# Kernel optimization log

Hardware: AMD Instinct MI355X
Metric: run time of the kernel (lower is better)

## Reference

```python
import jax, jax.numpy as jnp
import numpy as np

# 3x3 window roll offsets, row-major as in PatchShift2D.shift_content
SHIFTS = [(1, 1), (1, 0), (1, -1), (0, 1), (0, 0), (0, -1), (-1, 1), (-1, 0), (-1, -1)]
NUM_WIN = 9


def patch_shift(x, inv):
    # x: [B, T, H, W, C]; pad C up to multiple of 9 and H,W by 1, roll each
    # of the 9 channel groups by a distinct (h, w) offset, then crop back.
    B, T, H, W, C = x.shape
    Ch = int(np.ceil(C / NUM_WIN) * NUM_WIN)
    xp = jnp.pad(x, ((0, 0), (0, 0), (1, 1), (1, 1), (0, Ch - C)))
    m = -1 if inv else 1
    parts = jnp.split(xp, NUM_WIN, axis=-1)
    shifted = [jnp.roll(p, (m * sh, m * sw), axis=(2, 3))
               for p, (sh, sw) in zip(parts, SHIFTS)]
    return jnp.concatenate(shifted, axis=-1)[:, :, 1:H + 1, 1:W + 1, :C]


def _gelu(v):
    return jax.nn.gelu(v, approximate=False)  # torch nn.GELU default (erf)


def setup_inputs() -> dict:
    key = jax.random.key(0)
    ks = jax.random.split(key, 14)
    B, T, H, W, C = 2, 8, 56, 56, 512
    HID = 1024
    s = 0.02
    return {
        "x": jax.random.normal(ks[0], (B, T, H, W, C), dtype=jnp.float32),
        "fc_w": s * jax.random.normal(ks[1], (C, HID), dtype=jnp.float32),
        "fc_b": jnp.zeros((HID,), jnp.float32),
        "fc1_w": s * jax.random.normal(ks[2], (HID, C), dtype=jnp.float32),
        "fc1_b": jnp.zeros((C,), jnp.float32),
        "fc2_w": s * jax.random.normal(ks[3], (HID, C), dtype=jnp.float32),
        "fc2_b": jnp.zeros((C,), jnp.float32),
        "rw1_w": s * jax.random.normal(ks[4], (C, C // 4), dtype=jnp.float32),
        "rw1_b": jnp.zeros((C // 4,), jnp.float32),
        "rw2_w": s * jax.random.normal(ks[5], (C // 4, 2 * C), dtype=jnp.float32),
        "rw2_b": jnp.zeros((2 * C,), jnp.float32),
        "proj_w": s * jax.random.normal(ks[6], (C, C), dtype=jnp.float32),
        "proj_b": jnp.zeros((C,), jnp.float32),
    }


def reference(x, fc_w, fc_b, fc1_w, fc1_b, fc2_w, fc2_b,
              rw1_w, rw1_b, rw2_w, rw2_b, proj_w, proj_b):
    B, T, H, W, C = x.shape
    xh = _gelu(x @ fc_w + fc_b)                                  # [B,T,H,W,HID]
    h = patch_shift(_gelu(patch_shift(xh, False) @ fc1_w + fc1_b), True)  # [B,T,H,W,C]
    w = _gelu(xh @ fc2_w + fc2_b)                                 # [B,T,H,W,C]
    a = (h + w).mean(axis=(1, 2, 3))                              # [B,C]
    a = _gelu(a @ rw1_w + rw1_b) @ rw2_w + rw2_b                  # [B,2C]
    a = jax.nn.softmax(a.reshape(B, C, 2).transpose(2, 0, 1), axis=0)  # [2,B,C]
    a = a[:, :, None, None, None, :]                              # [2,B,1,1,1,C]
    out = h * a[0] + w * a[1]
    return out @ proj_w + proj_b
```

## Files before the change

kernel.cpp:

```cpp
#include <hip/hip_runtime.h>
#include <hip/hip_bf16.h>
#include <stdint.h>


typedef __attribute__((ext_vector_type(8))) short short8;
typedef __attribute__((ext_vector_type(4))) float floatx4;
typedef unsigned int uint;
typedef unsigned short ushort;

#define NTOK   50176
#define HWIMG  3136

__device__ __forceinline__ float gelu_exact(float v) {
    return 0.5f * v * (1.0f + erff(v * 0.70710678118654752440f));
}
__device__ __forceinline__ float gelu_fast(float v) {
    float u = v * (0.7978845608f + 0.0356774081f * v * v);
    return v * __builtin_amdgcn_rcpf(1.0f + __expf(-2.0f * u));
}

__device__ __forceinline__ int shift_h(int g) { return 1 - g / 3; }
__device__ __forceinline__ int shift_w(int g) { return 1 - g % 3; }

typedef const __attribute__((address_space(1))) uint* gas_ptr;
typedef __attribute__((address_space(3))) uint* las_ptr;

__device__ __forceinline__ void async_copy16(const void* g, void* l) {
    gas_ptr gp = (gas_ptr)(uintptr_t)g;
    las_ptr lp = (las_ptr)(uint32_t)(uintptr_t)l;
    __builtin_amdgcn_global_load_lds(gp, lp, 16, 0, 0);
}

template <int EPI, bool SHIFTA>
__global__ __launch_bounds__(256) void gemm_bt(
    const __hip_bfloat16* __restrict__ A,
    const __hip_bfloat16* __restrict__ Bt,
    const float* __restrict__ bias,
    void* __restrict__ Cout,
    float* __restrict__ ssum, int N, int K)
{
    __shared__ __align__(16) __hip_bfloat16 As[128 * 32];
    __shared__ __align__(16) __hip_bfloat16 Bs[128 * 32];

    const int t    = threadIdx.x;
    const int lane = t & 63;
    const int wave = t >> 6;
    const int wm   = wave >> 1;
    const int wn   = wave & 1;

    const int nbn  = gridDim.x;
    const int flat = blockIdx.y * nbn + blockIdx.x;
    const int xcd  = flat & 7;
    const int j    = flat >> 3;
    const int jd   = j / nbn;
    const int bm   = xcd * 49 + jd;
    const int bn   = j - jd * nbn;

    const int ar0 = bm * 128 + (t >> 2);
    const int ar1 = ar0 + 64;
    const int ac  = (t & 3) * 8;

    const __hip_bfloat16* ga0 = A  + (size_t)ar0 * K + ac;
    const __hip_bfloat16* ga1 = ga0 + (size_t)64 * K;
    const __hip_bfloat16* gb0 = Bt + (size_t)(bn * 128 + (t >> 2)) * K + ac;
    const __hip_bfloat16* gb1 = gb0 + (size_t)64 * K;
    __hip_bfloat16* la0 = &As[t * 8];
    __hip_bfloat16* la1 = &As[t * 8 + 2048];
    __hip_bfloat16* lb0 = &Bs[t * 8];
    __hip_bfloat16* lb1 = &Bs[t * 8 + 2048];

    int oh0 = 0, ow0 = 0, oh1 = 0, ow1 = 0;
    if (SHIFTA) {
        const int rem0 = ar0 % HWIMG, rem1 = ar1 % HWIMG;
        oh0 = rem0 / 56; ow0 = rem0 - oh0 * 56;
        oh1 = rem1 / 56; ow1 = rem1 - oh1 * 56;
    }

    floatx4 acc[4][4] = {};

    const int kq = (lane >> 4) * 8;
    const int ml = lane & 15;

    for (int k0 = 0; k0 < K; k0 += 32) {
        async_copy16(gb0, lb0);
        async_copy16(gb1, lb1);
        gb0 += 32; gb1 += 32;

        uint4 av0 = {0, 0, 0, 0}, av1 = {0, 0, 0, 0};
        if (SHIFTA) {
            const int c0 = k0 + ac;
            const int g  = c0 / 114;
            const int ge = (c0 + 7) / 114;
            if (g == ge) {
                const int sh = shift_h(g), sw = shift_w(g);
                const int off = sh * 56 + sw;
                if ((unsigned)(oh0 - sh) < 56u && (unsigned)(ow0 - sw) < 56u)
                    av0 = *(const uint4*)(A + (size_t)(ar0 - off) * K + c0);
                if ((unsigned)(oh1 - sh) < 56u && (unsigned)(ow1 - sw) < 56u)
                    av1 = *(const uint4*)(A + (size_t)(ar1 - off) * K + c0);
            } else {
                union { ushort us[8]; uint4 v; } p0, p1;
#pragma unroll
                for (int e = 0; e < 8; e++) {
                    const int c  = c0 + e;
                    const int gg = c / 114;
                    const int sh = shift_h(gg), sw = shift_w(gg);
                    const int off = sh * 56 + sw;
                    ushort v0 = 0, v1 = 0;
                    if ((unsigned)(oh0 - sh) < 56u && (unsigned)(ow0 - sw) < 56u)
                        v0 = *(const ushort*)(A + (size_t)(ar0 - off) * K + c);
                    if ((unsigned)(oh1 - sh) < 56u && (unsigned)(ow1 - sw) < 56u)
                        v1 = *(const ushort*)(A + (size_t)(ar1 - off) * K + c);
                    p0.us[e] = v0; p1.us[e] = v1;
                }
                av0 = p0.v; av1 = p1.v;
            }
        } else {
            async_copy16(ga0, la0);
            async_copy16(ga1, la1);
            ga0 += 32; ga1 += 32;
        }

        asm volatile("s_waitcnt vmcnt(0)" ::: "memory");
        if (SHIFTA) {
            *(uint4*)la0 = av0;
            *(uint4*)la1 = av1;
        }
        __syncthreads();

        short8 af[4], bf[4];
#pragma unroll
        for (int i = 0; i < 4; i++) {
            af[i] = *(const short8*)&As[(wm * 64 + i * 16 + ml) * 32 + kq];
            bf[i] = *(const short8*)&Bs[(wn * 64 + i * 16 + ml) * 32 + kq];
        }
#pragma unroll
        for (int mi = 0; mi < 4; mi++)
#pragma unroll
            for (int ni = 0; ni < 4; ni++)
                acc[mi][ni] = __builtin_amdgcn_mfma_f32_16x16x32_bf16(
                    af[mi], bf[ni], acc[mi][ni], 0, 0, 0);
        __syncthreads();
    }

    const int rq = (lane >> 4) * 4;

    int cols[4], gsh[4], gsw[4];
    float bv[4];
    float sum[4] = {0.f, 0.f, 0.f, 0.f};
#pragma unroll
    for (int ni = 0; ni < 4; ni++) {
        const int col = bn * 128 + wn * 64 + ni * 16 + ml;
        cols[ni] = col;
        bv[ni] = bias[col];
        if (EPI == 2) { const int g = col / 57; gsh[ni] = shift_h(g); gsw[ni] = shift_w(g); }
    }

#pragma unroll
    for (int mi = 0; mi < 4; mi++) {
        const int row0 = bm * 128 + wm * 64 + mi * 16 + rq;
        int phr[4], pwr[4];
        if (EPI == 2) {
            const int bt_ = row0 / HWIMG;
            const int rem = row0 - bt_ * HWIMG;
            const int ph0 = rem / 56;
            const int pw0 = rem - ph0 * 56;
#pragma unroll
            for (int r = 0; r < 4; r++) {
                int pw = pw0 + r, ph = ph0;
                if (pw >= 56) { pw -= 56; ph += 1; }
                if (ph >= 56) { ph = 0; }
                phr[r] = ph; pwr[r] = pw;
            }
        }
#pragma unroll
        for (int ni = 0; ni < 4; ni++) {
            const int col = cols[ni];
#pragma unroll
            for (int r = 0; r < 4; r++) {
                const int tok = row0 + r;
                float v = acc[mi][ni][r] + bv[ni];
                if (EPI != 0) v = gelu_fast(v);
                if (EPI == 0) {
                    ((float*)Cout)[(size_t)tok * N + col] = v;
                } else if (EPI == 1) {
                    ((__hip_bfloat16*)Cout)[(size_t)tok * N + col] = __float2bfloat16(v);
                } else if (EPI == 2) {
                    const int th = phr[r] - gsh[ni], tw = pwr[r] - gsw[ni];
                    if ((unsigned)th < 56u && (unsigned)tw < 56u) {
                        ((__hip_bfloat16*)Cout)[(size_t)(tok - gsh[ni] * 56 - gsw[ni]) * N + col]
                            = __float2bfloat16(v);
                        sum[ni] += v;
                    }
                } else {
                    ((__hip_bfloat16*)Cout)[(size_t)tok * N + col] = __float2bfloat16(v);
                    sum[ni] += v;
                }
            }
        }
    }

    if (EPI == 2 || EPI == 3) {
        const int b = (bm >= 196) ? 1 : 0;
#pragma unroll
        for (int ni = 0; ni < 4; ni++) {
            float s = sum[ni];
            s += __shfl_xor(s, 16, 64);
            s += __shfl_xor(s, 32, 64);
            if (lane < 16) atomicAdd(&ssum[b * 512 + cols[ni]], s);
        }
    }
}

template <int C, int GS, int SGN>
__global__ __launch_bounds__(256) void zero_holes(__hip_bfloat16* __restrict__ buf)
{
    const int i = blockIdx.x * 256 + threadIdx.x;
    const int c = i % C;
    const int p = i / C;
    const int bt = p / 220, fp = p % 220;
    int oh, ow;
    if (fp < 56)       { oh = 0;        ow = fp; }
    else if (fp < 112) { oh = 55;       ow = fp - 56; }
    else if (fp < 166) { oh = fp - 111; ow = 0; }
    else               { oh = fp - 165; ow = 55; }
    const int g = c / GS;
    const int ih = oh - SGN * shift_h(g);
    const int iw = ow - SGN * shift_w(g);
    if ((unsigned)ih >= 56u || (unsigned)iw >= 56u)
        buf[((size_t)(bt * HWIMG + oh * 56 + ow)) * C + c] = __float2bfloat16(0.0f);
}

__global__ __launch_bounds__(256) void cvt_x(const float4* __restrict__ x,
                                             __hip_bfloat16* __restrict__ xb)
{
    int i = blockIdx.x * 256 + threadIdx.x;
    float4 v = x[i];
    __hip_bfloat16 b0 = __float2bfloat16(v.x);
    __hip_bfloat16 b1 = __float2bfloat16(v.y);
    __hip_bfloat16 b2 = __float2bfloat16(v.z);
    __hip_bfloat16 b3 = __float2bfloat16(v.w);
    uint2 o;
    o.x = (uint)*(ushort*)&b0 | ((uint)*(ushort*)&b1 << 16);
    o.y = (uint)*(ushort*)&b2 | ((uint)*(ushort*)&b3 << 16);
    *(uint2*)&xb[(size_t)i * 4] = o;
}

__global__ __launch_bounds__(256) void prep_w(
    const float* __restrict__ fcw,  const float* __restrict__ fc1w,
    const float* __restrict__ fc2w, const float* __restrict__ projw,
    __hip_bfloat16* __restrict__ fcwT, __hip_bfloat16* __restrict__ fc1T,
    __hip_bfloat16* __restrict__ fc2T, __hip_bfloat16* __restrict__ projT)
{
    int i = blockIdx.x * 256 + threadIdx.x;
    if (i < 524288) {
        int n = i >> 9, k = i & 511;
        fcwT[i] = __float2bfloat16(fcw[k * 1024 + n]);
    } else if (i < 1048576) {
        int j = i - 524288;
        int n = j >> 10, k = j & 1023;
        fc1T[j] = __float2bfloat16(fc1w[k * 512 + n]);
    } else if (i < 1572864) {
        int j = i - 1048576;
        int n = j >> 10, k = j & 1023;
        fc2T[j] = __float2bfloat16(fc2w[k * 512 + n]);
    } else if (i < 1835008) {
        int j = i - 1572864;
        int n = j >> 9, k = j & 511;
        projT[j] = __float2bfloat16(projw[k * 512 + n]);
    }
}

__global__ __launch_bounds__(256) void tiny_mlp(
    const float* __restrict__ s0, const float* __restrict__ s1,
    const float* __restrict__ rw1_w, const float* __restrict__ rw1_b,
    const float* __restrict__ rw2_w, const float* __restrict__ rw2_b,
    float* __restrict__ a0, float* __restrict__ a1)
{
    __shared__ float mean[1024];
    __shared__ float z[256];
    __shared__ float av[2048];
    const int t = threadIdx.x;
    for (int i = t; i < 1024; i += 256)
        mean[i] = (s0[i] + s1[i]) * (1.0f / 25088.0f);
    __syncthreads();
    {
        const int b = t >> 7, j = t & 127;
        float acc = rw1_b[j];
        for (int cc = 0; cc < 512; cc++)
            acc += mean[b * 512 + cc] * rw1_w[cc * 128 + j];
        z[t] = gelu_exact(acc);
    }
    __syncthreads();
    for (int i = t; i < 2048; i += 256) {
        const int b = i >> 10, o = i & 1023;
        float acc = rw2_b[o];
        for (int j = 0; j < 128; j++)
            acc += z[b * 128 + j] * rw2_w[j * 1024 + o];
        av[i] = acc;
    }
    __syncthreads();
    for (int i = t; i < 1024; i += 256) {
        const int b = i >> 9, cc = i & 511;
        const float x0 = av[b * 1024 + 2 * cc];
        const float x1 = av[b * 1024 + 2 * cc + 1];
        const float m = fmaxf(x0, x1);
        const float e0 = expf(x0 - m), e1 = expf(x1 - m);
        const float inv = 1.0f / (e0 + e1);
        a0[i] = e0 * inv;
        a1[i] = e1 * inv;
    }
}

__device__ __forceinline__ float bf_lo(uint u) { return __uint_as_float(u << 16); }
__device__ __forceinline__ float bf_hi(uint u) { return __uint_as_float(u & 0xffff0000u); }
__device__ __forceinline__ uint pack_bf2(float lo, float hi) {
    __hip_bfloat16 a = __float2bfloat16(lo), b = __float2bfloat16(hi);
    return (uint)*(ushort*)&a | ((uint)*(ushort*)&b << 16);
}

__global__ __launch_bounds__(256) void combine(
    const uint4* __restrict__ hs4, const uint4* __restrict__ w4,
    const float* __restrict__ a0, const float* __restrict__ a1,
    uint4* __restrict__ hw4)
{
    const int i = blockIdx.x * 256 + threadIdx.x;
    const int ck = i & 63;
    const int tok = i >> 6;
    const int b = (tok >= 25088) ? 1 : 0;
    const float4* A0 = (const float4*)&a0[b * 512 + ck * 8];
    const float4* A1 = (const float4*)&a1[b * 512 + ck * 8];
    const float4 s0l = A0[0], s0h = A0[1];
    const float4 s1l = A1[0], s1h = A1[1];
    const uint4 h = hs4[i], w = w4[i];
    uint4 o;
    o.x = pack_bf2(bf_lo(h.x) * s0l.x + bf_lo(w.x) * s1l.x,
                   bf_hi(h.x) * s0l.y + bf_hi(w.x) * s1l.y);
    o.y = pack_bf2(bf_lo(h.y) * s0l.z + bf_lo(w.y) * s1l.z,
                   bf_hi(h.y) * s0l.w + bf_hi(w.y) * s1l.w);
    o.z = pack_bf2(bf_lo(h.z) * s0h.x + bf_lo(w.z) * s1h.x,
                   bf_hi(h.z) * s0h.y + bf_hi(w.z) * s1h.y);
    o.w = pack_bf2(bf_lo(h.w) * s0h.z + bf_lo(w.w) * s1h.z,
                   bf_hi(h.w) * s0h.w + bf_hi(w.w) * s1h.w);
    hw4[i] = o;
}

extern "C" void kernel_launch(void* const* d_in, const int* in_sizes, int n_in,
                              void* d_out, int out_size, void* d_ws, size_t ws_size,
                              hipStream_t stream)
{
    const float* x      = (const float*)d_in[0];
    const float* fc_w   = (const float*)d_in[1];
    const float* fc_b   = (const float*)d_in[2];
    const float* fc1_w  = (const float*)d_in[3];
    const float* fc1_b  = (const float*)d_in[4];
    const float* fc2_w  = (const float*)d_in[5];
    const float* fc2_b  = (const float*)d_in[6];
    const float* rw1_w  = (const float*)d_in[7];
    const float* rw1_b  = (const float*)d_in[8];
    const float* rw2_w  = (const float*)d_in[9];
    const float* rw2_b  = (const float*)d_in[10];
    const float* proj_w = (const float*)d_in[11];
    const float* proj_b = (const float*)d_in[12];

    uint8_t* ws = (uint8_t*)d_ws;
    __hip_bfloat16* xh  = (__hip_bfloat16*)(ws);
    __hip_bfloat16* xb  = (__hip_bfloat16*)(ws + 102760448);
    uint8_t* wt         = ws + 102760448 + 51380224;
    __hip_bfloat16* fcwT  = (__hip_bfloat16*)(wt);
    __hip_bfloat16* fc1T  = fcwT + 524288;
    __hip_bfloat16* fc2T  = fc1T + 524288;
    __hip_bfloat16* projT = fc2T + 524288;
    float* s0 = (float*)(wt + 3670016);
    float* s1 = s0 + 1024;
    float* a0 = s1 + 1024;
    float* a1 = a0 + 1024;

    __hip_bfloat16* wbuf = (__hip_bfloat16*)d_out;
    __hip_bfloat16* hs   = xb;
    __hip_bfloat16* hw   = xh;

    hipMemsetAsync(s0, 0, 8192, stream);

    cvt_x<<<25088, 256, 0, stream>>>((const float4*)x, xb);
    prep_w<<<7168, 256, 0, stream>>>(fc_w, fc1_w, fc2_w, proj_w, fcwT, fc1T, fc2T, projT);

    gemm_bt<1, false><<<dim3(8, 392), 256, 0, stream>>>(xb, fcwT, fc_b, xh, nullptr, 1024, 512);
    zero_holes<512, 57, -1><<<7040, 256, 0, stream>>>(hs);
    gemm_bt<2, true><<<dim3(4, 392), 256, 0, stream>>>(xh, fc1T, fc1_b, hs, s0, 512, 1024);
    gemm_bt<3, false><<<dim3(4, 392), 256, 0, stream>>>(xh, fc2T, fc2_b, wbuf, s1, 512, 1024);
    tiny_mlp<<<1, 256, 0, stream>>>(s0, s1, rw1_w, rw1_b, rw2_w, rw2_b, a0, a1);
    combine<<<12544, 256, 0, stream>>>((const uint4*)hs, (const uint4*)wbuf, a0, a1, (uint4*)hw);
    gemm_bt<0, false><<<dim3(4, 392), 256, 0, stream>>>(hw, projT, proj_b, d_out, nullptr, 512, 512);
}
```

Measured before the change: 621.3 us.

## Fuse fc1 and fc2 GEMMs into one kernel sharing the xh tile reads

Merges the shifted-A fc1 GEMM and the plain fc2 GEMM into a single kernel that loads the same xh rows once per k-step, in both shifted and unshifted form, and keeps two accumulator sets. The goal is to avoid reading the large xh activation twice from memory and to drop one launch. The cost is doubled accumulator registers (32 floatx4) and doubled LDS per block, which may lower occupancy or cause spills.

```diff
diff --git a/kernel.cpp b/kernel.cpp
--- a/kernel.cpp
+++ b/kernel.cpp
@@ -31,13 +31,12 @@
     __builtin_amdgcn_global_load_lds(gp, lp, 16, 0, 0);
 }
 
-template <int EPI, bool SHIFTA>
+template <int EPI>
 __global__ __launch_bounds__(256) void gemm_bt(
     const __hip_bfloat16* __restrict__ A,
     const __hip_bfloat16* __restrict__ Bt,
     const float* __restrict__ bias,
-    void* __restrict__ Cout,
-    float* __restrict__ ssum, int N, int K)
+    void* __restrict__ Cout, int N, int K)
 {
     __shared__ __align__(16) __hip_bfloat16 As[128 * 32];
     __shared__ __align__(16) __hip_bfloat16 Bs[128 * 32];
@@ -56,38 +55,128 @@
     const int bm   = xcd * 49 + jd;
     const int bn   = j - jd * nbn;
 
-    const int ar0 = bm * 128 + (t >> 2);
-    const int ar1 = ar0 + 64;
-    const int ac  = (t & 3) * 8;
-
-    const __hip_bfloat16* ga0 = A  + (size_t)ar0 * K + ac;
+    const __hip_bfloat16* ga0 = A  + (size_t)(bm * 128 + (t >> 2)) * K + (t & 3) * 8;
     const __hip_bfloat16* ga1 = ga0 + (size_t)64 * K;
-    const __hip_bfloat16* gb0 = Bt + (size_t)(bn * 128 + (t >> 2)) * K + ac;
+    const __hip_bfloat16* gb0 = Bt + (size_t)(bn * 128 + (t >> 2)) * K + (t & 3) * 8;
     const __hip_bfloat16* gb1 = gb0 + (size_t)64 * K;
     __hip_bfloat16* la0 = &As[t * 8];
     __hip_bfloat16* la1 = &As[t * 8 + 2048];
     __hip_bfloat16* lb0 = &Bs[t * 8];
     __hip_bfloat16* lb1 = &Bs[t * 8 + 2048];
 
-    int oh0 = 0, ow0 = 0, oh1 = 0, ow1 = 0;
-    if (SHIFTA) {
-        const int rem0 = ar0 % HWIMG, rem1 = ar1 % HWIMG;
-        oh0 = rem0 / 56; ow0 = rem0 - oh0 * 56;
-        oh1 = rem1 / 56; ow1 = rem1 - oh1 * 56;
-    }
-
     floatx4 acc[4][4] = {};
 
     const int kq = (lane >> 4) * 8;
     const int ml = lane & 15;
 
     for (int k0 = 0; k0 < K; k0 += 32) {
+        async_copy16(ga0, la0);
+        async_copy16(ga1, la1);
         async_copy16(gb0, lb0);
         async_copy16(gb1, lb1);
-        gb0 += 32; gb1 += 32;
+        ga0 += 32; ga1 += 32; gb0 += 32; gb1 += 32;
+        asm volatile("s_waitcnt vmcnt(0)" ::: "memory");
+        __syncthreads();
+
+        short8 af[4], bf[4];
+#pragma unroll
+        for (int i = 0; i < 4; i++) {
+            af[i] = *(const short8*)&As[(wm * 64 + i * 16 + ml) * 32 + kq];
+            bf[i] = *(const short8*)&Bs[(wn * 64 + i * 16 + ml) * 32 + kq];
+        }
+#pragma unroll
+        for (int mi = 0; mi < 4; mi++)
+#pragma unroll
+            for (int ni = 0; ni < 4; ni++)
+                acc[mi][ni] = __builtin_amdgcn_mfma_f32_16x16x32_bf16(
+                    af[mi], bf[ni], acc[mi][ni], 0, 0, 0);
+        __syncthreads();
+    }
+
+    const int rq = (lane >> 4) * 4;
+
+#pragma unroll
+    for (int mi = 0; mi < 4; mi++) {
+        const int row0 = bm * 128 + wm * 64 + mi * 16 + rq;
+#pragma unroll
+        for (int ni = 0; ni < 4; ni++) {
+            const int col = bn * 128 + wn * 64 + ni * 16 + ml;
+            const float bv = bias[col];
+#pragma unroll
+            for (int r = 0; r < 4; r++) {
+                const int tok = row0 + r;
+                float v = acc[mi][ni][r] + bv;
+                if (EPI == 0) {
+                    ((float*)Cout)[(size_t)tok * N + col] = v;
+                } else {
+                    v = gelu_fast(v);
+                    ((__hip_bfloat16*)Cout)[(size_t)tok * N + col] = __float2bfloat16(v);
+                }
+            }
+        }
+    }
+}
+
+__global__ __launch_bounds__(256) void gemm23(
+    const __hip_bfloat16* __restrict__ A,
+    const __hip_bfloat16* __restrict__ B1t,
+    const __hip_bfloat16* __restrict__ B2t,
+    const float* __restrict__ bias1, const float* __restrict__ bias2,
+    __hip_bfloat16* __restrict__ C1, __hip_bfloat16* __restrict__ C2,
+    float* __restrict__ s0, float* __restrict__ s1)
+{
+    const int N = 512, K = 1024;
+    __shared__ __align__(16) __hip_bfloat16 Ash[128 * 32];
+    __shared__ __align__(16) __hip_bfloat16 Aun[128 * 32];
+    __shared__ __align__(16) __hip_bfloat16 B1s[128 * 32];
+    __shared__ __align__(16) __hip_bfloat16 B2s[128 * 32];
+
+    const int t    = threadIdx.x;
+    const int lane = t & 63;
+    const int wave = t >> 6;
+    const int wm   = wave >> 1;
+    const int wn   = wave & 1;
+
+    const int nbn  = gridDim.x;
+    const int flat = blockIdx.y * nbn + blockIdx.x;
+    const int xcd  = flat & 7;
+    const int j    = flat >> 3;
+    const int jd   = j / nbn;
+    const int bm   = xcd * 49 + jd;
+    const int bn   = j - jd * nbn;
+
+    const int ar0 = bm * 128 + (t >> 2);
+    const int ar1 = ar0 + 64;
+    const int ac  = (t & 3) * 8;
+
+    const __hip_bfloat16* gau0 = A   + (size_t)ar0 * K + ac;
+    const __hip_bfloat16* gau1 = gau0 + (size_t)64 * K;
+    const __hip_bfloat16* gb10 = B1t + (size_t)(bn * 128 + (t >> 2)) * K + ac;
+    const __hip_bfloat16* gb11 = gb10 + (size_t)64 * K;
+    const __hip_bfloat16* gb20 = B2t + (size_t)(bn * 128 + (t >> 2)) * K + ac;
+    const __hip_bfloat16* gb21 = gb20 + (size_t)64 * K;
+
+    const int rem0 = ar0 % HWIMG, rem1 = ar1 % HWIMG;
+    const int oh0 = rem0 / 56, ow0 = rem0 - oh0 * 56;
+    const int oh1 = rem1 / 56, ow1 = rem1 - oh1 * 56;
+
+    floatx4 acch[4][4] = {};
+    floatx4 accw[4][4] = {};
+
+    const int kq = (lane >> 4) * 8;
+    const int ml = lane & 15;
+
+    for (int k0 = 0; k0 < K; k0 += 32) {
+        async_copy16(gau0, &Aun[t * 8]);
+        async_copy16(gau1, &Aun[t * 8 + 2048]);
+        async_copy16(gb10, &B1s[t * 8]);
+        async_copy16(gb11, &B1s[t * 8 + 2048]);
+        async_copy16(gb20, &B2s[t * 8]);
+        async_copy16(gb21, &B2s[t * 8 + 2048]);
+        gau0 += 32; gau1 += 32; gb10 += 32; gb11 += 32; gb20 += 32; gb21 += 32;
 
         uint4 av0 = {0, 0, 0, 0}, av1 = {0, 0, 0, 0};
-        if (SHIFTA) {
+        {
             const int c0 = k0 + ac;
             const int g  = c0 / 114;
             const int ge = (c0 + 7) / 114;
@@ -115,63 +204,65 @@
                 }
                 av0 = p0.v; av1 = p1.v;
             }
-        } else {
-            async_copy16(ga0, la0);
-            async_copy16(ga1, la1);
-            ga0 += 32; ga1 += 32;
         }
 
         asm volatile("s_waitcnt vmcnt(0)" ::: "memory");
-        if (SHIFTA) {
-            *(uint4*)la0 = av0;
-            *(uint4*)la1 = av1;
-        }
+        *(uint4*)&Ash[t * 8] = av0;
+        *(uint4*)&Ash[t * 8 + 2048] = av1;
         __syncthreads();
 
-        short8 af[4], bf[4];
+        short8 afs[4], afu[4], bf1[4], bf2[4];
 #pragma unroll
         for (int i = 0; i < 4; i++) {
-            af[i] = *(const short8*)&As[(wm * 64 + i * 16 + ml) * 32 + kq];
-            bf[i] = *(const short8*)&Bs[(wn * 64 + i * 16 + ml) * 32 + kq];
+            const int arow = (wm * 64 + i * 16 + ml) * 32 + kq;
+            const int brow = (wn * 64 + i * 16 + ml) * 32 + kq;
+            afs[i] = *(const short8*)&Ash[arow];
+            afu[i] = *(const short8*)&Aun[arow];
+            bf1[i] = *(const short8*)&B1s[brow];
+            bf2[i] = *(const short8*)&B2s[brow];
         }
 #pragma unroll
         for (int mi = 0; mi < 4; mi++)
 #pragma unroll
-            for (int ni = 0; ni < 4; ni++)
-                acc[mi][ni] = __builtin_amdgcn_mfma_f32_16x16x32_bf16(
-                    af[mi], bf[ni], acc[mi][ni], 0, 0, 0);
+            for (int ni = 0; ni < 4; ni++) {
+                acch[mi][ni] = __builtin_amdgcn_mfma_f32_16x16x32_bf16(
+                    afs[mi], bf1[ni], acch[mi][ni], 0, 0, 0);
+                accw[mi][ni] = __builtin_amdgcn_mfma_f32_16x16x32_bf16(
+                    afu[mi], bf2[ni], accw[mi][ni], 0, 0, 0);
+            }
         __syncthreads();
     }
 
     const int rq = (lane >> 4) * 4;
 
     int cols[4], gsh[4], gsw[4];
-    float bv[4];
-    float sum[4] = {0.f, 0.f, 0.f, 0.f};
+    float bv1[4], bv2[4];
+    float sumh[4] = {0.f, 0.f, 0.f, 0.f};
+    float sumw[4] = {0.f, 0.f, 0.f, 0.f};
 #pragma unroll
     for (int ni = 0; ni < 4; ni++) {
         const int col = bn * 128 + wn * 64 + ni * 16 + ml;
         cols[ni] = col;
-        bv[ni] = bias[col];
-        if (EPI == 2) { const int g = col / 57; gsh[ni] = shift_h(g); gsw[ni] = shift_w(g); }
+        bv1[ni] = bias1[col];
+        bv2[ni] = bias2[col];
+        const int g = col / 57;
+        gsh[ni] = shift_h(g); gsw[ni] = shift_w(g);
     }
 
 #pragma unroll
     for (int mi = 0; mi < 4; mi++) {
         const int row0 = bm * 128 + wm * 64 + mi * 16 + rq;
+        const int bt_ = row0 / HWIMG;
+        const int rem = row0 - bt_ * HWIMG;
+        const int ph0 = rem / 56;
+        const int pw0 = rem - ph0 * 56;
         int phr[4], pwr[4];
-        if (EPI == 2) {
-            const int bt_ = row0 / HWIMG;
-            const int rem = row0 - bt_ * HWIMG;
-            const int ph0 = rem / 56;
-            const int pw0 = rem - ph0 * 56;
-#pragma unroll
-            for (int r = 0; r < 4; r++) {
-                int pw = pw0 + r, ph = ph0;
-                if (pw >= 56) { pw -= 56; ph += 1; }
-                if (ph >= 56) { ph = 0; }
-                phr[r] = ph; pwr[r] = pw;
-            }
+#pragma unroll
+        for (int r = 0; r < 4; r++) {
+            int pw = pw0 + r, ph = ph0;
+            if (pw >= 56) { pw -= 56; ph += 1; }
+            if (ph >= 56) { ph = 0; }
+            phr[r] = ph; pwr[r] = pw;
         }
 #pragma unroll
         for (int ni = 0; ni < 4; ni++) {
@@ -179,35 +270,32 @@
 #pragma unroll
             for (int r = 0; r < 4; r++) {
                 const int tok = row0 + r;
-                float v = acc[mi][ni][r] + bv[ni];
-                if (EPI != 0) v = gelu_fast(v);
-                if (EPI == 0) {
-                    ((float*)Cout)[(size_t)tok * N + col] = v;
-                } else if (EPI == 1) {
-                    ((__hip_bfloat16*)Cout)[(size_t)tok * N + col] = __float2bfloat16(v);
-                } else if (EPI == 2) {
-                    const int th = phr[r] - gsh[ni], tw = pwr[r] - gsw[ni];
-                    if ((unsigned)th < 56u && (unsigned)tw < 56u) {
-                        ((__hip_bfloat16*)Cout)[(size_t)(tok - gsh[ni] * 56 - gsw[ni]) * N + col]
-                            = __float2bfloat16(v);
-                        sum[ni] += v;
-                    }
-                } else {
-                    ((__hip_bfloat16*)Cout)[(size_t)tok * N + col] = __float2bfloat16(v);
-                    sum[ni] += v;
+                float vw = gelu_fast(accw[mi][ni][r] + bv2[ni]);
+                C2[(size_t)tok * N + col] = __float2bfloat16(vw);
+                sumw[ni] += vw;
+                float vh = gelu_fast(acch[mi][ni][r] + bv1[ni]);
+                const int th = phr[r] - gsh[ni], tw = pwr[r] - gsw[ni];
+                if ((unsigned)th < 56u && (unsigned)tw < 56u) {
+                    C1[(size_t)(tok - gsh[ni] * 56 - gsw[ni]) * N + col]
+                        = __float2bfloat16(vh);
+                    sumh[ni] += vh;
                 }
             }
         }
     }
 
-    if (EPI == 2 || EPI == 3) {
-        const int b = (bm >= 196) ? 1 : 0;
-#pragma unroll
-        for (int ni = 0; ni < 4; ni++) {
-            float s = sum[ni];
-            s += __shfl_xor(s, 16, 64);
-            s += __shfl_xor(s, 32, 64);
-            if (lane < 16) atomicAdd(&ssum[b * 512 + cols[ni]], s);
+    const int b = (bm >= 196) ? 1 : 0;
+#pragma unroll
+    for (int ni = 0; ni < 4; ni++) {
+        float sh_ = sumh[ni];
+        sh_ += __shfl_xor(sh_, 16, 64);
+        sh_ += __shfl_xor(sh_, 32, 64);
+        float sw_ = sumw[ni];
+        sw_ += __shfl_xor(sw_, 16, 64);
+        sw_ += __shfl_xor(sw_, 32, 64);
+        if (lane < 16) {
+            atomicAdd(&s0[b * 512 + cols[ni]], sh_);
+            atomicAdd(&s1[b * 512 + cols[ni]], sw_);
         }
     }
 }
@@ -385,11 +473,11 @@
     cvt_x<<<25088, 256, 0, stream>>>((const float4*)x, xb);
     prep_w<<<7168, 256, 0, stream>>>(fc_w, fc1_w, fc2_w, proj_w, fcwT, fc1T, fc2T, projT);
 
-    gemm_bt<1, false><<<dim3(8, 392), 256, 0, stream>>>(xb, fcwT, fc_b, xh, nullptr, 1024, 512);
+    gemm_bt<1><<<dim3(8, 392), 256, 0, stream>>>(xb, fcwT, fc_b, xh, 1024, 512);
     zero_holes<512, 57, -1><<<7040, 256, 0, stream>>>(hs);
-    gemm_bt<2, true><<<dim3(4, 392), 256, 0, stream>>>(xh, fc1T, fc1_b, hs, s0, 512, 1024);
-    gemm_bt<3, false><<<dim3(4, 392), 256, 0, stream>>>(xh, fc2T, fc2_b, wbuf, s1, 512, 1024);
+    gemm23<<<dim3(4, 392), 256, 0, stream>>>(xh, fc1T, fc2T, fc1_b, fc2_b,
+                                             hs, wbuf, s0, s1);
     tiny_mlp<<<1, 256, 0, stream>>>(s0, s1, rw1_w, rw1_b, rw2_w, rw2_b, a0, a1);
     combine<<<12544, 256, 0, stream>>>((const uint4*)hs, (const uint4*)wbuf, a0, a1, (uint4*)hw);
-    gemm_bt<0, false><<<dim3(4, 392), 256, 0, stream>>>(hw, projT, proj_b, d_out, nullptr, 512, 512);
-}
+    gemm_bt<0><<<dim3(4, 392), 256, 0, stream>>>(hw, projT, proj_b, d_out, 512, 512);
+}
```

Measured after the change: 742.6 us. +19.5%, slower.

## Fuse input bf16 conversion and attention combine into GEMM A-operand loads

Applied to the files above, without the earlier changes.

The first GEMM now reads fp32 x directly and converts it to bf16 while staging into LDS, removing the separate conversion kernel and its intermediate buffer. When the workspace is large enough, the final projection GEMM builds its A tile on the fly as h*a0 + w*a1 from the two branch outputs, eliminating the combine kernel and the hw buffer round trip. Both paths replace async global-to-LDS copies with register loads plus ALU work, which may reduce load/compute overlap inside those GEMMs.

```diff
diff --git a/kernel.cpp b/kernel.cpp
--- a/kernel.cpp
+++ b/kernel.cpp
@@ -22,6 +22,13 @@
 __device__ __forceinline__ int shift_h(int g) { return 1 - g / 3; }
 __device__ __forceinline__ int shift_w(int g) { return 1 - g % 3; }
 
+__device__ __forceinline__ float bf_lo(uint u) { return __uint_as_float(u << 16); }
+__device__ __forceinline__ float bf_hi(uint u) { return __uint_as_float(u & 0xffff0000u); }
+__device__ __forceinline__ uint pack_bf2(float lo, float hi) {
+    __hip_bfloat16 a = __float2bfloat16(lo), b = __float2bfloat16(hi);
+    return (uint)*(ushort*)&a | ((uint)*(ushort*)&b << 16);
+}
+
 typedef const __attribute__((address_space(1))) uint* gas_ptr;
 typedef __attribute__((address_space(3))) uint* las_ptr;
 
@@ -31,11 +38,14 @@
     __builtin_amdgcn_global_load_lds(gp, lp, 16, 0, 0);
 }
 
-template <int EPI, bool SHIFTA>
+template <int EPI, int ASRC>
 __global__ __launch_bounds__(256) void gemm_bt(
-    const __hip_bfloat16* __restrict__ A,
+    const void* __restrict__ Av,
+    const __hip_bfloat16* __restrict__ A2,
     const __hip_bfloat16* __restrict__ Bt,
     const float* __restrict__ bias,
+    const float* __restrict__ sc0,
+    const float* __restrict__ sc1,
     void* __restrict__ Cout,
     float* __restrict__ ssum, int N, int K)
 {
@@ -56,11 +66,14 @@
     const int bm   = xcd * 49 + jd;
     const int bn   = j - jd * nbn;
 
+    const __hip_bfloat16* Ab = (const __hip_bfloat16*)Av;
+    const float*          Af = (const float*)Av;
+
     const int ar0 = bm * 128 + (t >> 2);
     const int ar1 = ar0 + 64;
     const int ac  = (t & 3) * 8;
 
-    const __hip_bfloat16* ga0 = A  + (size_t)ar0 * K + ac;
+    const __hip_bfloat16* ga0 = Ab + (size_t)ar0 * K + ac;
     const __hip_bfloat16* ga1 = ga0 + (size_t)64 * K;
     const __hip_bfloat16* gb0 = Bt + (size_t)(bn * 128 + (t >> 2)) * K + ac;
     const __hip_bfloat16* gb1 = gb0 + (size_t)64 * K;
@@ -70,11 +83,12 @@
     __hip_bfloat16* lb1 = &Bs[t * 8 + 2048];
 
     int oh0 = 0, ow0 = 0, oh1 = 0, ow1 = 0;
-    if (SHIFTA) {
+    if (ASRC == 3) {
         const int rem0 = ar0 % HWIMG, rem1 = ar1 % HWIMG;
         oh0 = rem0 / 56; ow0 = rem0 - oh0 * 56;
         oh1 = rem1 / 56; ow1 = rem1 - oh1 * 56;
     }
+    const int bsel = (ASRC == 2 && bm >= 196) ? 1 : 0;
 
     floatx4 acc[4][4] = {};
 
@@ -87,7 +101,46 @@
         gb0 += 32; gb1 += 32;
 
         uint4 av0 = {0, 0, 0, 0}, av1 = {0, 0, 0, 0};
-        if (SHIFTA) {
+        if (ASRC == 0) {
+            async_copy16(ga0, la0);
+            async_copy16(ga1, la1);
+            ga0 += 32; ga1 += 32;
+        } else if (ASRC == 1) {
+            const float* p0 = Af + (size_t)ar0 * K + k0 + ac;
+            const float* p1 = Af + (size_t)ar1 * K + k0 + ac;
+            const float4 f0 = *(const float4*)p0, f1 = *(const float4*)(p0 + 4);
+            const float4 f2 = *(const float4*)p1, f3 = *(const float4*)(p1 + 4);
+            av0.x = pack_bf2(f0.x, f0.y); av0.y = pack_bf2(f0.z, f0.w);
+            av0.z = pack_bf2(f1.x, f1.y); av0.w = pack_bf2(f1.z, f1.w);
+            av1.x = pack_bf2(f2.x, f2.y); av1.y = pack_bf2(f2.z, f2.w);
+            av1.z = pack_bf2(f3.x, f3.y); av1.w = pack_bf2(f3.z, f3.w);
+        } else if (ASRC == 2) {
+            const int c0 = k0 + ac;
+            const float4 s0l = *(const float4*)&sc0[bsel * 512 + c0];
+            const float4 s0h = *(const float4*)&sc0[bsel * 512 + c0 + 4];
+            const float4 s1l = *(const float4*)&sc1[bsel * 512 + c0];
+            const float4 s1h = *(const float4*)&sc1[bsel * 512 + c0 + 4];
+            const uint4 h0 = *(const uint4*)(Ab + (size_t)ar0 * K + c0);
+            const uint4 w0 = *(const uint4*)(A2 + (size_t)ar0 * K + c0);
+            const uint4 h1 = *(const uint4*)(Ab + (size_t)ar1 * K + c0);
+            const uint4 w1 = *(const uint4*)(A2 + (size_t)ar1 * K + c0);
+            av0.x = pack_bf2(bf_lo(h0.x) * s0l.x + bf_lo(w0.x) * s1l.x,
+                             bf_hi(h0.x) * s0l.y + bf_hi(w0.x) * s1l.y);
+            av0.y = pack_bf2(bf_lo(h0.y) * s0l.z + bf_lo(w0.y) * s1l.z,
+                             bf_hi(h0.y) * s0l.w + bf_hi(w0.y) * s1l.w);
+            av0.z = pack_bf2(bf_lo(h0.z) * s0h.x + bf_lo(w0.z) * s1h.x,
+                             bf_hi(h0.z) * s0h.y + bf_hi(w0.z) * s1h.y);
+            av0.w = pack_bf2(bf_lo(h0.w) * s0h.z + bf_lo(w0.w) * s1h.z,
+                             bf_hi(h0.w) * s0h.w + bf_hi(w0.w) * s1h.w);
+            av1.x = pack_bf2(bf_lo(h1.x) * s0l.x + bf_lo(w1.x) * s1l.x,
+                             bf_hi(h1.x) * s0l.y + bf_hi(w1.x) * s1l.y);
+            av1.y = pack_bf2(bf_lo(h1.y) * s0l.z + bf_lo(w1.y) * s1l.z,
+                             bf_hi(h1.y) * s0l.w + bf_hi(w1.y) * s1l.w);
+            av1.z = pack_bf2(bf_lo(h1.z) * s0h.x + bf_lo(w1.z) * s1h.x,
+                             bf_hi(h1.z) * s0h.y + bf_hi(w1.z) * s1h.y);
+            av1.w = pack_bf2(bf_lo(h1.w) * s0h.z + bf_lo(w1.w) * s1h.z,
+                             bf_hi(h1.w) * s0h.w + bf_hi(w1.w) * s1h.w);
+        } else {
             const int c0 = k0 + ac;
             const int g  = c0 / 114;
             const int ge = (c0 + 7) / 114;
@@ -95,9 +148,9 @@
                 const int sh = shift_h(g), sw = shift_w(g);
                 const int off = sh * 56 + sw;
                 if ((unsigned)(oh0 - sh) < 56u && (unsigned)(ow0 - sw) < 56u)
-                    av0 = *(const uint4*)(A + (size_t)(ar0 - off) * K + c0);
+                    av0 = *(const uint4*)(Ab + (size_t)(ar0 - off) * K + c0);
                 if ((unsigned)(oh1 - sh) < 56u && (unsigned)(ow1 - sw) < 56u)
-                    av1 = *(const uint4*)(A + (size_t)(ar1 - off) * K + c0);
+                    av1 = *(const uint4*)(Ab + (size_t)(ar1 - off) * K + c0);
             } else {
                 union { ushort us[8]; uint4 v; } p0, p1;
 #pragma unroll
@@ -108,21 +161,17 @@
                     const int off = sh * 56 + sw;
                     ushort v0 = 0, v1 = 0;
                     if ((unsigned)(oh0 - sh) < 56u && (unsigned)(ow0 - sw) < 56u)
-                        v0 = *(const ushort*)(A + (size_t)(ar0 - off) * K + c);
+                        v0 = *(const ushort*)(Ab + (size_t)(ar0 - off) * K + c);
                     if ((unsigned)(oh1 - sh) < 56u && (unsigned)(ow1 - sw) < 56u)
-                        v1 = *(const ushort*)(A + (size_t)(ar1 - off) * K + c);
+                        v1 = *(const ushort*)(Ab + (size_t)(ar1 - off) * K + c);
                     p0.us[e] = v0; p1.us[e] = v1;
                 }
                 av0 = p0.v; av1 = p1.v;
             }
-        } else {
-            async_copy16(ga0, la0);
-            async_copy16(ga1, la1);
-            ga0 += 32; ga1 += 32;
         }
 
         asm volatile("s_waitcnt vmcnt(0)" ::: "memory");
-        if (SHIFTA) {
+        if (ASRC != 0) {
             *(uint4*)la0 = av0;
             *(uint4*)la1 = av1;
         }
@@ -231,21 +280,6 @@
         buf[((size_t)(bt * HWIMG + oh * 56 + ow)) * C + c] = __float2bfloat16(0.0f);
 }
 
-__global__ __launch_bounds__(256) void cvt_x(const float4* __restrict__ x,
-                                             __hip_bfloat16* __restrict__ xb)
-{
-    int i = blockIdx.x * 256 + threadIdx.x;
-    float4 v = x[i];
-    __hip_bfloat16 b0 = __float2bfloat16(v.x);
-    __hip_bfloat16 b1 = __float2bfloat16(v.y);
-    __hip_bfloat16 b2 = __float2bfloat16(v.z);
-    __hip_bfloat16 b3 = __float2bfloat16(v.w);
-    uint2 o;
-    o.x = (uint)*(ushort*)&b0 | ((uint)*(ushort*)&b1 << 16);
-    o.y = (uint)*(ushort*)&b2 | ((uint)*(ushort*)&b3 << 16);
-    *(uint2*)&xb[(size_t)i * 4] = o;
-}
-
 __global__ __launch_bounds__(256) void prep_w(
     const float* __restrict__ fcw,  const float* __restrict__ fc1w,
     const float* __restrict__ fc2w, const float* __restrict__ projw,
@@ -310,13 +344,6 @@
         a0[i] = e0 * inv;
         a1[i] = e1 * inv;
     }
-}
-
-__device__ __forceinline__ float bf_lo(uint u) { return __uint_as_float(u << 16); }
-__device__ __forceinline__ float bf_hi(uint u) { return __uint_as_float(u & 0xffff0000u); }
-__device__ __forceinline__ uint pack_bf2(float lo, float hi) {
-    __hip_bfloat16 a = __float2bfloat16(lo), b = __float2bfloat16(hi);
-    return (uint)*(ushort*)&a | ((uint)*(ushort*)&b << 16);
 }
 
 __global__ __launch_bounds__(256) void combine(
@@ -365,7 +392,7 @@
 
     uint8_t* ws = (uint8_t*)d_ws;
     __hip_bfloat16* xh  = (__hip_bfloat16*)(ws);
-    __hip_bfloat16* xb  = (__hip_bfloat16*)(ws + 102760448);
+    __hip_bfloat16* hs  = (__hip_bfloat16*)(ws + 102760448);
     uint8_t* wt         = ws + 102760448 + 51380224;
     __hip_bfloat16* fcwT  = (__hip_bfloat16*)(wt);
     __hip_bfloat16* fc1T  = fcwT + 524288;
@@ -376,20 +403,31 @@
     float* a0 = s1 + 1024;
     float* a1 = a0 + 1024;
 
-    __hip_bfloat16* wbuf = (__hip_bfloat16*)d_out;
-    __hip_bfloat16* hs   = xb;
-    __hip_bfloat16* hw   = xh;
+    const bool fused4 = (ws_size >= 209207296ull);
+    __hip_bfloat16* w_ = fused4 ? (__hip_bfloat16*)(ws + 157827072)
+                                : (__hip_bfloat16*)d_out;
+    __hip_bfloat16* hw = xh;
 
     hipMemsetAsync(s0, 0, 8192, stream);
 
-    cvt_x<<<25088, 256, 0, stream>>>((const float4*)x, xb);
+    zero_holes<512, 57, -1><<<7040, 256, 0, stream>>>(hs);
     prep_w<<<7168, 256, 0, stream>>>(fc_w, fc1_w, fc2_w, proj_w, fcwT, fc1T, fc2T, projT);
 
-    gemm_bt<1, false><<<dim3(8, 392), 256, 0, stream>>>(xb, fcwT, fc_b, xh, nullptr, 1024, 512);
-    zero_holes<512, 57, -1><<<7040, 256, 0, stream>>>(hs);
-    gemm_bt<2, true><<<dim3(4, 392), 256, 0, stream>>>(xh, fc1T, fc1_b, hs, s0, 512, 1024);
-    gemm_bt<3, false><<<dim3(4, 392), 256, 0, stream>>>(xh, fc2T, fc2_b, wbuf, s1, 512, 1024);
+    gemm_bt<1, 1><<<dim3(8, 392), 256, 0, stream>>>(
+        x, nullptr, fcwT, fc_b, nullptr, nullptr, xh, nullptr, 1024, 512);
+    gemm_bt<2, 3><<<dim3(4, 392), 256, 0, stream>>>(
+        xh, nullptr, fc1T, fc1_b, nullptr, nullptr, hs, s0, 512, 1024);
+    gemm_bt<3, 0><<<dim3(4, 392), 256, 0, stream>>>(
+        xh, nullptr, fc2T, fc2_b, nullptr, nullptr, w_, s1, 512, 1024);
     tiny_mlp<<<1, 256, 0, stream>>>(s0, s1, rw1_w, rw1_b, rw2_w, rw2_b, a0, a1);
-    combine<<<12544, 256, 0, stream>>>((const uint4*)hs, (const uint4*)wbuf, a0, a1, (uint4*)hw);
-    gemm_bt<0, false><<<dim3(4, 392), 256, 0, stream>>>(hw, projT, proj_b, d_out, nullptr, 512, 512);
-}
+
+    if (fused4) {
+        gemm_bt<0, 2><<<dim3(4, 392), 256, 0, stream>>>(
+            hs, w_, projT, proj_b, a0, a1, d_out, nullptr, 512, 512);
+    } else {
+        combine<<<12544, 256, 0, stream>>>(
+            (const uint4*)hs, (const uint4*)w_, a0, a1, (uint4*)hw);
+        gemm_bt<0, 0><<<dim3(4, 392), 256, 0, stream>>>(
+            hw, nullptr, projT, proj_b, nullptr, nullptr, d_out, nullptr, 512, 512);
+    }
+}
```

New measurement: 663.8 us. +6.8%, slower.

## Double-buffer LDS tiles in non-shifted GEMM path to overlap loads with MFMA

Applied to the files above, without the earlier changes.

For the non-shifted GEMM variants, the A and B LDS tiles are now double-buffered. The next K-tile's async global-to-LDS copies are issued before waiting on the current tile, using a partial vmcnt wait. This is meant to hide global load latency behind the MFMA work, which the single-buffer loop exposed by waiting for all loads every iteration. It doubles LDS use for those variants, which may lower occupancy; the shifted-A path is left unchanged.

```diff
diff --git a/kernel.cpp b/kernel.cpp
--- a/kernel.cpp
+++ b/kernel.cpp
@@ -39,8 +39,9 @@
     void* __restrict__ Cout,
     float* __restrict__ ssum, int N, int K)
 {
-    __shared__ __align__(16) __hip_bfloat16 As[128 * 32];
-    __shared__ __align__(16) __hip_bfloat16 Bs[128 * 32];
+    constexpr int NBUF = SHIFTA ? 1 : 2;
+    __shared__ __align__(16) __hip_bfloat16 As[NBUF * 128 * 32];
+    __shared__ __align__(16) __hip_bfloat16 Bs[NBUF * 128 * 32];
 
     const int t    = threadIdx.x;
     const int lane = t & 63;
@@ -64,83 +65,118 @@
     const __hip_bfloat16* ga1 = ga0 + (size_t)64 * K;
     const __hip_bfloat16* gb0 = Bt + (size_t)(bn * 128 + (t >> 2)) * K + ac;
     const __hip_bfloat16* gb1 = gb0 + (size_t)64 * K;
-    __hip_bfloat16* la0 = &As[t * 8];
-    __hip_bfloat16* la1 = &As[t * 8 + 2048];
-    __hip_bfloat16* lb0 = &Bs[t * 8];
-    __hip_bfloat16* lb1 = &Bs[t * 8 + 2048];
-
-    int oh0 = 0, ow0 = 0, oh1 = 0, ow1 = 0;
-    if (SHIFTA) {
-        const int rem0 = ar0 % HWIMG, rem1 = ar1 % HWIMG;
-        oh0 = rem0 / 56; ow0 = rem0 - oh0 * 56;
-        oh1 = rem1 / 56; ow1 = rem1 - oh1 * 56;
-    }
 
     floatx4 acc[4][4] = {};
 
     const int kq = (lane >> 4) * 8;
     const int ml = lane & 15;
 
-    for (int k0 = 0; k0 < K; k0 += 32) {
-        async_copy16(gb0, lb0);
-        async_copy16(gb1, lb1);
-        gb0 += 32; gb1 += 32;
-
-        uint4 av0 = {0, 0, 0, 0}, av1 = {0, 0, 0, 0};
-        if (SHIFTA) {
-            const int c0 = k0 + ac;
-            const int g  = c0 / 114;
-            const int ge = (c0 + 7) / 114;
-            if (g == ge) {
-                const int sh = shift_h(g), sw = shift_w(g);
-                const int off = sh * 56 + sw;
-                if ((unsigned)(oh0 - sh) < 56u && (unsigned)(ow0 - sw) < 56u)
-                    av0 = *(const uint4*)(A + (size_t)(ar0 - off) * K + c0);
-                if ((unsigned)(oh1 - sh) < 56u && (unsigned)(ow1 - sw) < 56u)
-                    av1 = *(const uint4*)(A + (size_t)(ar1 - off) * K + c0);
+    if constexpr (!SHIFTA) {
+        auto stage = [&](int buf) {
+            __hip_bfloat16* lA = &As[buf * 4096 + t * 8];
+            __hip_bfloat16* lB = &Bs[buf * 4096 + t * 8];
+            async_copy16(ga0, lA);
+            async_copy16(ga1, lA + 2048);
+            async_copy16(gb0, lB);
+            async_copy16(gb1, lB + 2048);
+            ga0 += 32; ga1 += 32; gb0 += 32; gb1 += 32;
+        };
+
+        const int nt = K >> 5;
+        stage(0);
+        for (int tt = 0; tt < nt; ++tt) {
+            const int cur = tt & 1;
+            if (tt + 1 < nt) {
+                stage(cur ^ 1);
+                asm volatile("s_waitcnt vmcnt(4)" ::: "memory");
             } else {
-                union { ushort us[8]; uint4 v; } p0, p1;
-#pragma unroll
-                for (int e = 0; e < 8; e++) {
-                    const int c  = c0 + e;
-                    const int gg = c / 114;
-                    const int sh = shift_h(gg), sw = shift_w(gg);
+                asm volatile("s_waitcnt vmcnt(0)" ::: "memory");
+            }
+            __builtin_amdgcn_s_barrier();
+            asm volatile("" ::: "memory");
+
+            const int ab = cur * 4096;
+            short8 af[4], bf[4];
+#pragma unroll
+            for (int i = 0; i < 4; i++) {
+                af[i] = *(const short8*)&As[ab + (wm * 64 + i * 16 + ml) * 32 + kq];
+                bf[i] = *(const short8*)&Bs[ab + (wn * 64 + i * 16 + ml) * 32 + kq];
+            }
+#pragma unroll
+            for (int mi = 0; mi < 4; mi++)
+#pragma unroll
+                for (int ni = 0; ni < 4; ni++)
+                    acc[mi][ni] = __builtin_amdgcn_mfma_f32_16x16x32_bf16(
+                        af[mi], bf[ni], acc[mi][ni], 0, 0, 0);
+
+            asm volatile("" ::: "memory");
+            __builtin_amdgcn_s_barrier();
+        }
+    } else {
+        __hip_bfloat16* la0 = &As[t * 8];
+        __hip_bfloat16* la1 = &As[t * 8 + 2048];
+        __hip_bfloat16* lb0 = &Bs[t * 8];
+        __hip_bfloat16* lb1 = &Bs[t * 8 + 2048];
+
+        const int rem0 = ar0 % HWIMG, rem1 = ar1 % HWIMG;
+        const int oh0 = rem0 / 56, ow0 = rem0 - oh0 * 56;
+        const int oh1 = rem1 / 56, ow1 = rem1 - oh1 * 56;
+
+        for (int k0 = 0; k0 < K; k0 += 32) {
+            async_copy16(gb0, lb0);
+            async_copy16(gb1, lb1);
+            gb0 += 32; gb1 += 32;
+
+            uint4 av0 = {0, 0, 0, 0}, av1 = {0, 0, 0, 0};
+            {
+                const int c0 = k0 + ac;
+                const int g  = c0 / 114;
+                const int ge = (c0 + 7) / 114;
+                if (g == ge) {
+                    const int sh = shift_h(g), sw = shift_w(g);
                     const int off = sh * 56 + sw;
-                    ushort v0 = 0, v1 = 0;
                     if ((unsigned)(oh0 - sh) < 56u && (unsigned)(ow0 - sw) < 56u)
-                        v0 = *(const ushort*)(A + (size_t)(ar0 - off) * K + c);
+                        av0 = *(const uint4*)(A + (size_t)(ar0 - off) * K + c0);
                     if ((unsigned)(oh1 - sh) < 56u && (unsigned)(ow1 - sw) < 56u)
-                        v1 = *(const ushort*)(A + (size_t)(ar1 - off) * K + c);
-                    p0.us[e] = v0; p1.us[e] = v1;
+                        av1 = *(const uint4*)(A + (size_t)(ar1 - off) * K + c0);
+                } else {
+                    union { ushort us[8]; uint4 v; } p0, p1;
+#pragma unroll
+                    for (int e = 0; e < 8; e++) {
+                        const int c  = c0 + e;
+                        const int gg = c / 114;
+                        const int sh = shift_h(gg), sw = shift_w(gg);
+                        const int off = sh * 56 + sw;
+                        ushort v0 = 0, v1 = 0;
+                        if ((unsigned)(oh0 - sh) < 56u && (unsigned)(ow0 - sw) < 56u)
+                            v0 = *(const ushort*)(A + (size_t)(ar0 - off) * K + c);
+                        if ((unsigned)(oh1 - sh) < 56u && (unsigned)(ow1 - sw) < 56u)
+                            v1 = *(const ushort*)(A + (size_t)(ar1 - off) * K + c);
+                        p0.us[e] = v0; p1.us[e] = v1;
+                    }
+                    av0 = p0.v; av1 = p1.v;
                 }
-                av0 = p0.v; av1 = p1.v;
-            }
-        } else {
-            async_copy16(ga0, la0);
-            async_copy16(ga1, la1);
-            ga0 += 32; ga1 += 32;
-        }
-
-        asm volatile("s_waitcnt vmcnt(0)" ::: "memory");
-        if (SHIFTA) {
+            }
+
+            asm volatile("s_waitcnt vmcnt(0)" ::: "memory");
             *(uint4*)la0 = av0;
             *(uint4*)la1 = av1;
+            __syncthreads();
+
+            short8 af[4], bf[4];
+#pragma unroll
+            for (int i = 0; i < 4; i++) {
+                af[i] = *(const short8*)&As[(wm * 64 + i * 16 + ml) * 32 + kq];
+                bf[i] = *(const short8*)&Bs[(wn * 64 + i * 16 + ml) * 32 + kq];
+            }
+#pragma unroll
+            for (int mi = 0; mi < 4; mi++)
+#pragma unroll
+                for (int ni = 0; ni < 4; ni++)
+                    acc[mi][ni] = __builtin_amdgcn_mfma_f32_16x16x32_bf16(
+                        af[mi], bf[ni], acc[mi][ni], 0, 0, 0);
+            __syncthreads();
         }
-        __syncthreads();
-
-        short8 af[4], bf[4];
-#pragma unroll
-        for (int i = 0; i < 4; i++) {
-            af[i] = *(const short8*)&As[(wm * 64 + i * 16 + ml) * 32 + kq];
-            bf[i] = *(const short8*)&Bs[(wn * 64 + i * 16 + ml) * 32 + kq];
-        }
-#pragma unroll
-        for (int mi = 0; mi < 4; mi++)
-#pragma unroll
-            for (int ni = 0; ni < 4; ni++)
-                acc[mi][ni] = __builtin_amdgcn_mfma_f32_16x16x32_bf16(
-                    af[mi], bf[ni], acc[mi][ni], 0, 0, 0);
-        __syncthreads();
     }
 
     const int rq = (lane >> 4) * 4;
```

New measurement: 575.0 us. -7.4%, faster.
